# Kernel optimization log

Hardware: AMD Instinct MI355X
Metric: run time of the kernel (lower is better)

Reference implementation:

```python
import jax, jax.numpy as jnp
import numpy as np

D_MODEL = 1024
N_HEADS = 16
N_KV = 4
HEAD_DIM = D_MODEL // N_HEADS  # 64
EPS = 1e-5
THETA = 10000.0


def _rope_tables(S):
    half = HEAD_DIM // 2
    inv_freq = 1.0 / (THETA ** (jnp.arange(half, dtype=jnp.float32) / half))
    t = jnp.arange(S, dtype=jnp.float32)
    f = t[:, None] * inv_freq[None, :]  # [S, half]
    return jnp.cos(f), jnp.sin(f)


def _apply_rope(x, cos, sin):
    # x: [B, H, S, D]
    half = x.shape[-1] // 2
    x1, x2 = x[..., :half], x[..., half:]
    c = cos[None, None, :, :]
    s = sin[None, None, :, :]
    return jnp.concatenate([x1 * c - x2 * s, x1 * s + x2 * c], axis=-1)


def _rmsnorm(x, scale):
    rms = jnp.sqrt(jnp.mean(x * x, axis=-1, keepdims=True) + EPS)
    return x / rms * scale


def setup_inputs() -> dict:
    key = jax.random.key(0)
    ks = jax.random.split(key, 4)
    B, S = 2, 2048
    x = jax.random.normal(ks[0], (B, S, D_MODEL), dtype=jnp.float32)
    Wq = jax.random.normal(ks[1], (D_MODEL, D_MODEL), dtype=jnp.float32) * 0.02
    Wkv = jax.random.normal(ks[2], (D_MODEL, 2 * N_KV * HEAD_DIM), dtype=jnp.float32) * 0.02
    Wo = jax.random.normal(ks[3], (D_MODEL, D_MODEL), dtype=jnp.float32) * 0.02
    q_scale = jnp.ones((HEAD_DIM,), dtype=jnp.float32)
    k_scale = jnp.ones((HEAD_DIM,), dtype=jnp.float32)
    return {"x": x, "Wq": Wq, "Wkv": Wkv, "Wo": Wo,
            "q_scale": q_scale, "k_scale": k_scale}


def reference(x, Wq, Wkv, Wo, q_scale, k_scale):
    B, S, D = x.shape
    groups = N_HEADS // N_KV  # GQA group size

    # projections
    q = (x @ Wq).reshape(B, S, N_HEADS, HEAD_DIM).transpose(0, 2, 1, 3)  # [B,H,S,d]
    kv = x @ Wkv
    k, v = jnp.split(kv, 2, axis=-1)
    k = k.reshape(B, S, N_KV, HEAD_DIM).transpose(0, 2, 1, 3)  # [B,Hkv,S,d]
    v = v.reshape(B, S, N_KV, HEAD_DIM).transpose(0, 2, 1, 3)

    # per-head QK-RMSNorm (before RoPE, as in the torch module)
    q = _rmsnorm(q, q_scale)
    k = _rmsnorm(k, k_scale)

    # RoPE
    cos, sin = _rope_tables(S)
    q = _apply_rope(q, cos, sin)
    k = _apply_rope(k, cos, sin)

    # causal GQA attention (equivalent to SDPA with enable_gqa=True)
    qg = q.reshape(B, N_KV, groups, S, HEAD_DIM)
    scale = 1.0 / np.sqrt(HEAD_DIM).astype(np.float32)
    scores = jnp.einsum('bkgsd,bktd->bkgst', qg, k) * scale  # [B,Hkv,g,S,S]
    causal = jnp.tril(jnp.ones((S, S), dtype=bool))
    scores = jnp.where(causal[None, None, None], scores, -jnp.inf)
    attn = jax.nn.softmax(scores, axis=-1)
    out = jnp.einsum('bkgst,bktd->bkgsd', attn, v)
    out = out.reshape(B, N_HEADS, S, HEAD_DIM).transpose(0, 2, 1, 3).reshape(B, S, D)
    return out @ Wo
```

## Files before the change

kernel.cpp:

```cpp
#include <hip/hip_runtime.h>

#define S_LEN 2048
#define BATCH 2
#define DM    1024
#define NH    16
#define NKV   4
#define HD    64
#define MROWS (BATCH * S_LEN)
#define NQKV  1536

typedef __attribute__((ext_vector_type(8))) short bf16x8;
typedef __attribute__((ext_vector_type(4))) short s16x4;
typedef __attribute__((ext_vector_type(4))) float f32x4;
typedef __attribute__((ext_vector_type(4))) int i32x4;

__device__ __forceinline__ unsigned short f2bf(float f) {
  unsigned int u = __float_as_uint(f);
  u += 0x7FFF + ((u >> 16) & 1);
  return (unsigned short)(u >> 16);
}

__device__ __forceinline__ void gload_lds16(const unsigned short* g, unsigned short* l) {
  __builtin_amdgcn_global_load_lds((const __attribute__((address_space(1))) void*)g,
                                   (__attribute__((address_space(3))) void*)l, 16, 0, 0);
}
__device__ __forceinline__ void gload_lds4(const unsigned short* g, unsigned short* l) {
  __builtin_amdgcn_global_load_lds((const __attribute__((address_space(1))) void*)g,
                                   (__attribute__((address_space(3))) void*)l, 4, 0, 0);
}

__global__ __launch_bounds__(256) void prep_kernel(const float* __restrict__ x,
                                                   unsigned short* __restrict__ xb,
                                                   const float* __restrict__ Wq,
                                                   const float* __restrict__ Wkv,
                                                   const float* __restrict__ Wo,
                                                   unsigned short* __restrict__ wt1,
                                                   unsigned short* __restrict__ wot) {
  __shared__ float tile[64][65];
  int bid = blockIdx.x;
  int t = threadIdx.x;
  if (bid < 4096) {
    int i = (bid * 256 + t) * 4;
    float4 v = *reinterpret_cast<const float4*>(x + i);
    xb[i + 0] = f2bf(v.x);
    xb[i + 1] = f2bf(v.y);
    xb[i + 2] = f2bf(v.z);
    xb[i + 3] = f2bf(v.w);
    return;
  }
  bid -= 4096;
  const float* in;
  unsigned short* out;
  int C, bx, by;
  if (bid < 256) { in = Wq; out = wt1; C = 1024; bx = bid & 15; by = bid >> 4; }
  else if (bid < 384) { int k = bid - 256; in = Wkv; out = wt1 + 1024 * 1024; C = 512; bx = k & 7; by = k >> 3; }
  else { int k = bid - 384; in = Wo; out = wot; C = 1024; bx = k & 15; by = k >> 4; }
  const int R = 1024;
  int r0 = by * 64, c0 = bx * 64;
  int rl = t >> 2, cs = (t & 3) * 16;
#pragma unroll
  for (int k = 0; k < 4; ++k) {
    float4 v = *reinterpret_cast<const float4*>(in + (size_t)(r0 + rl) * C + c0 + cs + 4 * k);
    tile[rl][cs + 4 * k + 0] = v.x;
    tile[rl][cs + 4 * k + 1] = v.y;
    tile[rl][cs + 4 * k + 2] = v.z;
    tile[rl][cs + 4 * k + 3] = v.w;
  }
  __syncthreads();
  int cl = t >> 2, rs = (t & 3) * 16;
  bf16x8 v0, v1;
#pragma unroll
  for (int i = 0; i < 8; ++i) v0[i] = (short)f2bf(tile[rs + i][cl]);
#pragma unroll
  for (int i = 0; i < 8; ++i) v1[i] = (short)f2bf(tile[rs + 8 + i][cl]);
  unsigned short* dst = out + (size_t)(c0 + cl) * R + r0 + rs;
  *reinterpret_cast<bf16x8*>(dst) = v0;
  *reinterpret_cast<bf16x8*>(dst + 8) = v1;
}

__global__ __launch_bounds__(256) void gemm1_fused(const unsigned short* __restrict__ A,
                                                   const unsigned short* __restrict__ BT,
                                                   const float* __restrict__ q_scale,
                                                   const float* __restrict__ k_scale,
                                                   unsigned short* __restrict__ qb,
                                                   unsigned short* __restrict__ kbuf,
                                                   unsigned short* __restrict__ vt,
                                                   int K) {
  __shared__ __align__(16) unsigned short As[2][128 * 64];
  __shared__ __align__(16) unsigned short Bs[2][64 * 64];
  int bx = blockIdx.x;
  int row0 = blockIdx.y * 128, col0 = bx * 64;
  int t = threadIdx.x;
  int w = t >> 6, lane = t & 63, quad = lane >> 4, l16 = lane & 15;
  int srow = lane >> 3;
  int scol = (lane & 7) * 8;

  f32x4 acc[2][4];
#pragma unroll
  for (int i = 0; i < 2; ++i)
#pragma unroll
    for (int j = 0; j < 4; ++j) acc[i][j] = (f32x4){0.f, 0.f, 0.f, 0.f};

  auto stage = [&](int k0, int buf) {
#pragma unroll
    for (int j = 0; j < 4; ++j)
      gload_lds16(A + (size_t)(row0 + w * 32 + j * 8 + srow) * K + k0 + scol,
                  &As[buf][(w * 32 + j * 8) * 64]);
#pragma unroll
    for (int j = 0; j < 2; ++j)
      gload_lds16(BT + (size_t)(col0 + w * 16 + j * 8 + srow) * K + k0 + scol,
                  &Bs[buf][(w * 16 + j * 8) * 64]);
  };

  stage(0, 0);
  int cur = 0;
  for (int k0 = 0; k0 < K; k0 += 64) {
    __syncthreads();
    if (k0 + 64 < K) stage(k0 + 64, cur ^ 1);
#pragma unroll
    for (int ks = 0; ks < 2; ++ks) {
      bf16x8 af[2], bfr[4];
#pragma unroll
      for (int i = 0; i < 2; ++i)
        af[i] = *reinterpret_cast<const bf16x8*>(&As[cur][(w * 32 + i * 16 + l16) * 64 + ks * 32 + quad * 8]);
#pragma unroll
      for (int j = 0; j < 4; ++j)
        bfr[j] = *reinterpret_cast<const bf16x8*>(&Bs[cur][(j * 16 + l16) * 64 + ks * 32 + quad * 8]);
#pragma unroll
      for (int i = 0; i < 2; ++i)
#pragma unroll
        for (int j = 0; j < 4; ++j)
          acc[i][j] = __builtin_amdgcn_mfma_f32_16x16x32_bf16(af[i], bfr[j], acc[i][j], 0, 0, 0);
    }
    cur ^= 1;
  }

  if (bx < 20) {
    const float* scale = (bx < 16) ? q_scale : k_scale;
    float post = (bx < 16) ? 1.0f : 0.125f * 1.44269504088896f;
    float sc0 = scale[l16], sc1 = scale[16 + l16], sc2 = scale[32 + l16], sc3 = scale[48 + l16];
    float invf0 = exp2f((float)l16 * (-13.2877123795495f / 32.0f));
    float invf1 = exp2f((float)(l16 + 16) * (-13.2877123795495f / 32.0f));
#pragma unroll
    for (int i = 0; i < 2; ++i)
#pragma unroll
      for (int rg = 0; rg < 4; ++rg) {
        int row = row0 + w * 32 + i * 16 + quad * 4 + rg;
        int b = row >> 11, s = row & 2047;
        float v0 = acc[i][0][rg], v1 = acc[i][1][rg], v2 = acc[i][2][rg], v3 = acc[i][3][rg];
        float ss = v0 * v0 + v1 * v1 + v2 * v2 + v3 * v3;
        ss += __shfl_xor(ss, 1, 64);
        ss += __shfl_xor(ss, 2, 64);
        ss += __shfl_xor(ss, 4, 64);
        ss += __shfl_xor(ss, 8, 64);
        float inv_rms = 1.0f / sqrtf(ss * (1.0f / 64.0f) + 1e-5f);
        float n0 = v0 * inv_rms * sc0, n1 = v1 * inv_rms * sc1;
        float n2 = v2 * inv_rms * sc2, n3 = v3 * inv_rms * sc3;
        float f0 = (float)s * invf0, f1 = (float)s * invf1;
        float c0 = __cosf(f0), s0 = __sinf(f0), c1 = __cosf(f1), s1 = __sinf(f1);
        float o0 = (n0 * c0 - n2 * s0) * post;
        float o1 = (n1 * c1 - n3 * s1) * post;
        float o2 = (n0 * s0 + n2 * c0) * post;
        float o3 = (n1 * s1 + n3 * c1) * post;
        unsigned short* dst = (bx < 16)
            ? qb + ((size_t)(b * NH + bx) * S_LEN + s) * HD
            : kbuf + ((size_t)(b * NKV + (bx - 16)) * S_LEN + s) * HD;
        dst[l16] = f2bf(o0);
        dst[16 + l16] = f2bf(o1);
        dst[32 + l16] = f2bf(o2);
        dst[48 + l16] = f2bf(o3);
      }
  } else {
    int kvh = bx - 20;
    int b = row0 >> 11;
    unsigned short* vbase = vt + (size_t)(b * NKV + kvh) * HD * S_LEN;
#pragma unroll
    for (int i = 0; i < 2; ++i) {
      int s0 = (row0 & 2047) + w * 32 + i * 16 + quad * 4;
#pragma unroll
      for (int j = 0; j < 4; ++j) {
        int d = j * 16 + l16;
        s16x4 pv;
#pragma unroll
        for (int rg = 0; rg < 4; ++rg) pv[rg] = (short)f2bf(acc[i][j][rg]);
        *reinterpret_cast<s16x4*>(vbase + (size_t)d * S_LEN + s0) = pv;
      }
    }
  }
}

#define CH 136
#define TILE_SH (32 * CH)
__global__ __launch_bounds__(256, 4) void attn_kernel(const unsigned short* __restrict__ qb,
                                                      const unsigned short* __restrict__ kbuf,
                                                      const unsigned short* __restrict__ vt,
                                                      unsigned short* __restrict__ Opart,
                                                      float* __restrict__ lpart) {
  __shared__ __align__(16) unsigned short Ks[2][TILE_SH];
  __shared__ __align__(16) unsigned short Vs[2][TILE_SH];
  const size_t OZ = (size_t)BATCH * NH * S_LEN * HD;
  const size_t LZ = (size_t)BATCH * NH * S_LEN;
  int t32 = 63 - (int)(blockIdx.x >> 4);
  int sub = blockIdx.x & 15;
  int z = sub & 1;
  int bkv = sub >> 1;
  int b = bkv >> 2, kvh = bkv & 3;
  int w = threadIdx.x >> 6;
  int h = kvh * 4 + w;
  int lane = threadIdx.x & 63;
  int quad = lane >> 4, l16 = lane & 15;
  int qa = t32 * 32 + l16;
  const unsigned short* Q = qb + (size_t)(b * NH + h) * S_LEN * HD;
  const unsigned short* Kh = kbuf + (size_t)(b * NKV + kvh) * S_LEN * HD;
  const unsigned short* Vh = vt + (size_t)(b * NKV + kvh) * HD * S_LEN;

  bf16x8 bqa0 = *reinterpret_cast<const bf16x8*>(Q + (size_t)qa * HD + quad * 8);
  bf16x8 bqa1 = *reinterpret_cast<const bf16x8*>(Q + (size_t)qa * HD + 32 + quad * 8);
  bf16x8 bqb0 = *reinterpret_cast<const bf16x8*>(Q + (size_t)(qa + 16) * HD + quad * 8);
  bf16x8 bqb1 = *reinterpret_cast<const bf16x8*>(Q + (size_t)(qa + 16) * HD + 32 + quad * 8);

  bf16x8 ones;
#pragma unroll
  for (int i = 0; i < 8; ++i) ones[i] = (short)0x3F80;

  f32x4 ot[2][4];
#pragma unroll
  for (int gq = 0; gq < 2; ++gq)
#pragma unroll
    for (int i = 0; i < 4; ++i) ot[gq][i] = (f32x4){0.f, 0.f, 0.f, 0.f};
  f32x4 ol[2] = {(f32x4){0.f, 0.f, 0.f, 0.f}, (f32x4){0.f, 0.f, 0.f, 0.f}};

  int n = (t32 >> 1) + 1;

  auto stage = [&](int kbase, int dbuf) {
    const unsigned short* kg = Kh + (size_t)(kbase + w * 16) * HD + lane * 2;
    const unsigned short* vg = Vh + (size_t)(w * 16 + (lane >> 5)) * S_LEN + kbase + (lane & 31) * 2;
    unsigned short* kl = &Ks[dbuf][(w * 8) * CH];
    unsigned short* vl = &Vs[dbuf][(w * 8) * CH];
#pragma unroll
    for (int c = 0; c < 8; ++c) {
      gload_lds4(kg + (size_t)(2 * c) * HD, kl + c * CH);
      gload_lds4(vg + (size_t)(2 * c) * S_LEN, vl + c * CH);
    }
  };

  if (z < n) {
    stage(z << 6, 0);
    __syncthreads();

    for (int kb = z; kb < n; kb += 2) {
      int dbuf = (kb >> 1) & 1;
      bool diag = (kb == n - 1);
      if (kb + 2 < n) stage((kb + 2) << 6, dbuf ^ 1);
      int kbase = kb << 6;
      const unsigned short* Kd = Ks[dbuf];
      const unsigned short* Vd = Vs[dbuf];

      f32x4 sa[4], sb[4];
#pragma unroll
      for (int km = 0; km < 4; ++km) {
        int kk = 32 * (km >> 1) + 4 * (km & 1) + 8 * (l16 >> 2) + (l16 & 3);
        int base = (kk >> 1) * CH + (kk & 1) * 64;
        bf16x8 k0 = *reinterpret_cast<const bf16x8*>(&Kd[base + quad * 8]);
        bf16x8 k1 = *reinterpret_cast<const bf16x8*>(&Kd[base + 32 + quad * 8]);
        f32x4 s = {0.f, 0.f, 0.f, 0.f};
        s = __builtin_amdgcn_mfma_f32_16x16x32_bf16(k0, bqa0, s, 0, 0, 0);
        s = __builtin_amdgcn_mfma_f32_16x16x32_bf16(k1, bqa1, s, 0, 0, 0);
        sa[km] = s;
        f32x4 s2 = {0.f, 0.f, 0.f, 0.f};
        s2 = __builtin_amdgcn_mfma_f32_16x16x32_bf16(k0, bqb0, s2, 0, 0, 0);
        s2 = __builtin_amdgcn_mfma_f32_16x16x32_bf16(k1, bqb1, s2, 0, 0, 0);
        sb[km] = s2;
      }
      if (diag) {
#pragma unroll
        for (int km = 0; km < 4; ++km)
#pragma unroll
          for (int rg = 0; rg < 4; ++rg) {
            int key = kbase + 32 * (km >> 1) + 8 * quad + 4 * (km & 1) + rg;
            if (key > qa) sa[km][rg] = -1e30f;
            if (key > qa + 16) sb[km][rg] = -1e30f;
          }
      }
      unsigned int pk[4][2], qk[4][2];
#pragma unroll
      for (int km = 0; km < 4; ++km) {
        float a0 = exp2f(sa[km][0]), a1 = exp2f(sa[km][1]);
        float a2 = exp2f(sa[km][2]), a3 = exp2f(sa[km][3]);
        pk[km][0] = __builtin_amdgcn_perm(__float_as_uint(a1), __float_as_uint(a0), 0x07060302);
        pk[km][1] = __builtin_amdgcn_perm(__float_as_uint(a3), __float_as_uint(a2), 0x07060302);
        float b0 = exp2f(sb[km][0]), b1 = exp2f(sb[km][1]);
        float b2 = exp2f(sb[km][2]), b3 = exp2f(sb[km][3]);
        qk[km][0] = __builtin_amdgcn_perm(__float_as_uint(b1), __float_as_uint(b0), 0x07060302);
        qk[km][1] = __builtin_amdgcn_perm(__float_as_uint(b3), __float_as_uint(b2), 0x07060302);
      }
      i32x4 wa0 = {(int)pk[0][0], (int)pk[0][1], (int)pk[1][0], (int)pk[1][1]};
      i32x4 wa1 = {(int)pk[2][0], (int)pk[2][1], (int)pk[3][0], (int)pk[3][1]};
      i32x4 wb0 = {(int)qk[0][0], (int)qk[0][1], (int)qk[1][0], (int)qk[1][1]};
      i32x4 wb1 = {(int)qk[2][0], (int)qk[2][1], (int)qk[3][0], (int)qk[3][1]};
      bf16x8 pa0 = *reinterpret_cast<bf16x8*>(&wa0);
      bf16x8 pa1 = *reinterpret_cast<bf16x8*>(&wa1);
      bf16x8 pb0 = *reinterpret_cast<bf16x8*>(&wb0);
      bf16x8 pb1 = *reinterpret_cast<bf16x8*>(&wb1);
      ol[0] = __builtin_amdgcn_mfma_f32_16x16x32_bf16(ones, pa0, ol[0], 0, 0, 0);
      ol[0] = __builtin_amdgcn_mfma_f32_16x16x32_bf16(ones, pa1, ol[0], 0, 0, 0);
      ol[1] = __builtin_amdgcn_mfma_f32_16x16x32_bf16(ones, pb0, ol[1], 0, 0, 0);
      ol[1] = __builtin_amdgcn_mfma_f32_16x16x32_bf16(ones, pb1, ol[1], 0, 0, 0);
#pragma unroll
      for (int dm = 0; dm < 4; ++dm) {
        int ch = dm * 8 + (l16 >> 1);
        int base = ch * CH + (l16 & 1) * 64;
        bf16x8 v0 = *reinterpret_cast<const bf16x8*>(&Vd[base + quad * 8]);
        bf16x8 v1 = *reinterpret_cast<const bf16x8*>(&Vd[base + 32 + quad * 8]);
        ot[0][dm] = __builtin_amdgcn_mfma_f32_16x16x32_bf16(v0, pa0, ot[0][dm], 0, 0, 0);
        ot[0][dm] = __builtin_amdgcn_mfma_f32_16x16x32_bf16(v1, pa1, ot[0][dm], 0, 0, 0);
        ot[1][dm] = __builtin_amdgcn_mfma_f32_16x16x32_bf16(v0, pb0, ot[1][dm], 0, 0, 0);
        ot[1][dm] = __builtin_amdgcn_mfma_f32_16x16x32_bf16(v1, pb1, ot[1][dm], 0, 0, 0);
      }
      __syncthreads();
    }
  }

  unsigned short* Oz = Opart + (size_t)z * OZ;
  float* lz = lpart + (size_t)z * LZ;
#pragma unroll
  for (int gq = 0; gq < 2; ++gq) {
    size_t base = ((size_t)(b * NH + h) * S_LEN + qa + gq * 16) * HD;
#pragma unroll
    for (int dm = 0; dm < 4; ++dm) {
      s16x4 pv;
#pragma unroll
      for (int rg = 0; rg < 4; ++rg) pv[rg] = (short)f2bf(ot[gq][dm][rg]);
      *reinterpret_cast<s16x4*>(Oz + base + dm * 16 + quad * 4) = pv;
    }
  }
  if (quad == 0) {
    size_t lb = (size_t)(b * NH + h) * S_LEN + t32 * 32 + l16;
    lz[lb] = ol[0][0];
    lz[lb + 16] = ol[1][0];
  }
}

__global__ __launch_bounds__(256) void attn_combine_kernel(const unsigned short* __restrict__ Opart,
                                                           const float* __restrict__ lpart,
                                                           unsigned short* __restrict__ ctx) {
  const size_t OZ = (size_t)BATCH * NH * S_LEN * HD;
  const size_t LZ = (size_t)BATCH * NH * S_LEN;
  int i8 = blockIdx.x * 256 + threadIdx.x;
  size_t i = (size_t)i8 * 8;
  int row = i8 >> 3;
  bf16x8 a = *reinterpret_cast<const bf16x8*>(Opart + i);
  bf16x8 c = *reinterpret_cast<const bf16x8*>(Opart + OZ + i);
  float inv = 1.0f / (lpart[row] + lpart[LZ + row]);
  int q = row & 2047;
  int bh = row >> 11;
  int b = bh >> 4, h = bh & 15;
  int d0 = (i8 & 7) * 8;
  bf16x8 o;
#pragma unroll
  for (int k = 0; k < 8; ++k) {
    float fa = __uint_as_float(((unsigned int)(unsigned short)a[k]) << 16);
    float fc = __uint_as_float(((unsigned int)(unsigned short)c[k]) << 16);
    o[k] = (short)f2bf((fa + fc) * inv);
  }
  *reinterpret_cast<bf16x8*>(ctx + ((size_t)(b * S_LEN + q)) * DM + h * HD + d0) = o;
}

__global__ __launch_bounds__(256) void gemm_bt_n64(const unsigned short* __restrict__ A,
                                                   const unsigned short* __restrict__ BT,
                                                   float* __restrict__ C,
                                                   int M, int N, int K) {
  __shared__ __align__(16) unsigned short As[2][128 * 64];
  __shared__ __align__(16) unsigned short Bs[2][64 * 64];
  int row0 = blockIdx.y * 128, col0 = blockIdx.x * 64;
  int t = threadIdx.x;
  int w = t >> 6, lane = t & 63, quad = lane >> 4, l16 = lane & 15;
  int srow = lane >> 3;
  int scol = (lane & 7) * 8;

  f32x4 acc[2][4];
#pragma unroll
  for (int i = 0; i < 2; ++i)
#pragma unroll
    for (int j = 0; j < 4; ++j) acc[i][j] = (f32x4){0.f, 0.f, 0.f, 0.f};

  auto stage = [&](int k0, int buf) {
#pragma unroll
    for (int j = 0; j < 4; ++j)
      gload_lds16(A + (size_t)(row0 + w * 32 + j * 8 + srow) * K + k0 + scol,
                  &As[buf][(w * 32 + j * 8) * 64]);
#pragma unroll
    for (int j = 0; j < 2; ++j)
      gload_lds16(BT + (size_t)(col0 + w * 16 + j * 8 + srow) * K + k0 + scol,
                  &Bs[buf][(w * 16 + j * 8) * 64]);
  };

  stage(0, 0);
  int cur = 0;
  for (int k0 = 0; k0 < K; k0 += 64) {
    __syncthreads();
    if (k0 + 64 < K) stage(k0 + 64, cur ^ 1);
#pragma unroll
    for (int ks = 0; ks < 2; ++ks) {
      bf16x8 af[2], bfr[4];
#pragma unroll
      for (int i = 0; i < 2; ++i)
        af[i] = *reinterpret_cast<const bf16x8*>(&As[cur][(w * 32 + i * 16 + l16) * 64 + ks * 32 + quad * 8]);
#pragma unroll
      for (int j = 0; j < 4; ++j)
        bfr[j] = *reinterpret_cast<const bf16x8*>(&Bs[cur][(j * 16 + l16) * 64 + ks * 32 + quad * 8]);
#pragma unroll
      for (int i = 0; i < 2; ++i)
#pragma unroll
        for (int j = 0; j < 4; ++j)
          acc[i][j] = __builtin_amdgcn_mfma_f32_16x16x32_bf16(af[i], bfr[j], acc[i][j], 0, 0, 0);
    }
    cur ^= 1;
  }
#pragma unroll
  for (int i = 0; i < 2; ++i)
#pragma unroll
    for (int j = 0; j < 4; ++j) {
      int row = row0 + w * 32 + i * 16 + quad * 4;
      float* Cptr = C + (size_t)row * N + col0 + j * 16 + l16;
#pragma unroll
      for (int rg = 0; rg < 4; ++rg) Cptr[(size_t)rg * N] = acc[i][j][rg];
    }
}

extern "C" void kernel_launch(void* const* d_in, const int* in_sizes, int n_in,
                              void* d_out, int out_size, void* d_ws, size_t ws_size,
                              hipStream_t stream) {
  const float* x = (const float*)d_in[0];
  const float* Wq = (const float*)d_in[1];
  const float* Wkv = (const float*)d_in[2];
  const float* Wo = (const float*)d_in[3];
  const float* q_scale = (const float*)d_in[4];
  const float* k_scale = (const float*)d_in[5];
  float* out = (float*)d_out;

  char* ws = (char*)d_ws;
  size_t off = 0;
  auto alloc = [&](size_t bytes) {
    void* p = ws + off;
    off += (bytes + 255) & ~(size_t)255;
    return p;
  };
  unsigned short* xb = (unsigned short*)alloc((size_t)MROWS * DM * 2);
  unsigned short* wt1 = (unsigned short*)alloc((size_t)NQKV * DM * 2);
  unsigned short* wot = (unsigned short*)alloc((size_t)DM * DM * 2);
  unsigned short* qb = (unsigned short*)alloc((size_t)BATCH * NH * S_LEN * HD * 2);
  unsigned short* kbuf = (unsigned short*)alloc((size_t)BATCH * NKV * S_LEN * HD * 2);
  unsigned short* vt = (unsigned short*)alloc((size_t)BATCH * NKV * HD * S_LEN * 2);
  unsigned short* ctx = (unsigned short*)alloc((size_t)MROWS * DM * 2);
  unsigned short* Opart = (unsigned short*)alloc(2 * (size_t)BATCH * NH * S_LEN * HD * 2);
  float* lpart = (float*)alloc(2 * (size_t)BATCH * NH * S_LEN * 4);

  prep_kernel<<<4736, 256, 0, stream>>>(x, xb, Wq, Wkv, Wo, wt1, wot);

  gemm1_fused<<<dim3(NQKV / 64, MROWS / 128), 256, 0, stream>>>(xb, wt1, q_scale, k_scale,
                                                                qb, kbuf, vt, DM);

  attn_kernel<<<1024, 256, 0, stream>>>(qb, kbuf, vt, Opart, lpart);
  attn_combine_kernel<<<(BATCH * NH * S_LEN * HD / 8) / 256, 256, 0, stream>>>(Opart, lpart, ctx);

  gemm_bt_n64<<<dim3(DM / 64, MROWS / 128), 256, 0, stream>>>(ctx, wot, out, MROWS, DM, DM);
}
```

Measured before the change: 171.9 us.

## Drop split-K attention and fuse normalization into attention kernel epilogue

The attention kernel no longer splits each query tile's key range across two blocks. Each block now walks all key blocks with a single double-buffered pipeline and writes the normalized context directly, so the separate combine kernel and the partial O/l buffers go away. Blocks are ordered to pair heavy and light causal tiles (descending t32 for the first half, ascending for the second). The cost is half as many blocks (512) with longer serial loops per block, and launch bounds are relaxed to 2 blocks per SM, which could reduce parallelism on a large GPU.

Result: slower. 177.6 us (+3.3%).

```diff
diff --git a/kernel.cpp b/kernel.cpp
--- a/kernel.cpp
+++ b/kernel.cpp
@@ -191,19 +191,16 @@
 
 #define CH 136
 #define TILE_SH (32 * CH)
-__global__ __launch_bounds__(256, 4) void attn_kernel(const unsigned short* __restrict__ qb,
+__global__ __launch_bounds__(256, 2) void attn_kernel(const unsigned short* __restrict__ qb,
                                                       const unsigned short* __restrict__ kbuf,
                                                       const unsigned short* __restrict__ vt,
-                                                      unsigned short* __restrict__ Opart,
-                                                      float* __restrict__ lpart) {
+                                                      unsigned short* __restrict__ ctx) {
   __shared__ __align__(16) unsigned short Ks[2][TILE_SH];
   __shared__ __align__(16) unsigned short Vs[2][TILE_SH];
-  const size_t OZ = (size_t)BATCH * NH * S_LEN * HD;
-  const size_t LZ = (size_t)BATCH * NH * S_LEN;
-  int t32 = 63 - (int)(blockIdx.x >> 4);
-  int sub = blockIdx.x & 15;
-  int z = sub & 1;
-  int bkv = sub >> 1;
+  int bid = (int)blockIdx.x;
+  int u = bid >> 3;
+  int t32 = (bid < 256) ? (63 - 2 * u) : (2 * (u - 32));
+  int bkv = bid & 7;
   int b = bkv >> 2, kvh = bkv & 3;
   int w = threadIdx.x >> 6;
   int h = kvh * 4 + w;
@@ -244,126 +241,94 @@
     }
   };
 
-  if (z < n) {
-    stage(z << 6, 0);
+  stage(0, 0);
+  __syncthreads();
+
+  for (int kb = 0; kb < n; ++kb) {
+    int dbuf = kb & 1;
+    bool diag = (kb == n - 1);
+    if (kb + 1 < n) stage((kb + 1) << 6, dbuf ^ 1);
+    int kbase = kb << 6;
+    const unsigned short* Kd = Ks[dbuf];
+    const unsigned short* Vd = Vs[dbuf];
+
+    f32x4 sa[4], sb[4];
+#pragma unroll
+    for (int km = 0; km < 4; ++km) {
+      int kk = 32 * (km >> 1) + 4 * (km & 1) + 8 * (l16 >> 2) + (l16 & 3);
+      int base = (kk >> 1) * CH + (kk & 1) * 64;
+      bf16x8 k0 = *reinterpret_cast<const bf16x8*>(&Kd[base + quad * 8]);
+      bf16x8 k1 = *reinterpret_cast<const bf16x8*>(&Kd[base + 32 + quad * 8]);
+      f32x4 s = {0.f, 0.f, 0.f, 0.f};
+      s = __builtin_amdgcn_mfma_f32_16x16x32_bf16(k0, bqa0, s, 0, 0, 0);
+      s = __builtin_amdgcn_mfma_f32_16x16x32_bf16(k1, bqa1, s, 0, 0, 0);
+      sa[km] = s;
+      f32x4 s2 = {0.f, 0.f, 0.f, 0.f};
+      s2 = __builtin_amdgcn_mfma_f32_16x16x32_bf16(k0, bqb0, s2, 0, 0, 0);
+      s2 = __builtin_amdgcn_mfma_f32_16x16x32_bf16(k1, bqb1, s2, 0, 0, 0);
+      sb[km] = s2;
+    }
+    if (diag) {
+#pragma unroll
+      for (int km = 0; km < 4; ++km)
+#pragma unroll
+        for (int rg = 0; rg < 4; ++rg) {
+          int key = kbase + 32 * (km >> 1) + 8 * quad + 4 * (km & 1) + rg;
+          if (key > qa) sa[km][rg] = -1e30f;
+          if (key > qa + 16) sb[km][rg] = -1e30f;
+        }
+    }
+    unsigned int pk[4][2], qk[4][2];
+#pragma unroll
+    for (int km = 0; km < 4; ++km) {
+      float a0 = exp2f(sa[km][0]), a1 = exp2f(sa[km][1]);
+      float a2 = exp2f(sa[km][2]), a3 = exp2f(sa[km][3]);
+      pk[km][0] = __builtin_amdgcn_perm(__float_as_uint(a1), __float_as_uint(a0), 0x07060302);
+      pk[km][1] = __builtin_amdgcn_perm(__float_as_uint(a3), __float_as_uint(a2), 0x07060302);
+      float b0 = exp2f(sb[km][0]), b1 = exp2f(sb[km][1]);
+      float b2 = exp2f(sb[km][2]), b3 = exp2f(sb[km][3]);
+      qk[km][0] = __builtin_amdgcn_perm(__float_as_uint(b1), __float_as_uint(b0), 0x07060302);
+      qk[km][1] = __builtin_amdgcn_perm(__float_as_uint(b3), __float_as_uint(b2), 0x07060302);
+    }
+    i32x4 wa0 = {(int)pk[0][0], (int)pk[0][1], (int)pk[1][0], (int)pk[1][1]};
+    i32x4 wa1 = {(int)pk[2][0], (int)pk[2][1], (int)pk[3][0], (int)pk[3][1]};
+    i32x4 wb0 = {(int)qk[0][0], (int)qk[0][1], (int)qk[1][0], (int)qk[1][1]};
+    i32x4 wb1 = {(int)qk[2][0], (int)qk[2][1], (int)qk[3][0], (int)qk[3][1]};
+    bf16x8 pa0 = *reinterpret_cast<bf16x8*>(&wa0);
+    bf16x8 pa1 = *reinterpret_cast<bf16x8*>(&wa1);
+    bf16x8 pb0 = *reinterpret_cast<bf16x8*>(&wb0);
+    bf16x8 pb1 = *reinterpret_cast<bf16x8*>(&wb1);
+    ol[0] = __builtin_amdgcn_mfma_f32_16x16x32_bf16(ones, pa0, ol[0], 0, 0, 0);
+    ol[0] = __builtin_amdgcn_mfma_f32_16x16x32_bf16(ones, pa1, ol[0], 0, 0, 0);
+    ol[1] = __builtin_amdgcn_mfma_f32_16x16x32_bf16(ones, pb0, ol[1], 0, 0, 0);
+    ol[1] = __builtin_amdgcn_mfma_f32_16x16x32_bf16(ones, pb1, ol[1], 0, 0, 0);
+#pragma unroll
+    for (int dm = 0; dm < 4; ++dm) {
+      int ch = dm * 8 + (l16 >> 1);
+      int base = ch * CH + (l16 & 1) * 64;
+      bf16x8 v0 = *reinterpret_cast<const bf16x8*>(&Vd[base + quad * 8]);
+      bf16x8 v1 = *reinterpret_cast<const bf16x8*>(&Vd[base + 32 + quad * 8]);
+      ot[0][dm] = __builtin_amdgcn_mfma_f32_16x16x32_bf16(v0, pa0, ot[0][dm], 0, 0, 0);
+      ot[0][dm] = __builtin_amdgcn_mfma_f32_16x16x32_bf16(v1, pa1, ot[0][dm], 0, 0, 0);
+      ot[1][dm] = __builtin_amdgcn_mfma_f32_16x16x32_bf16(v0, pb0, ot[1][dm], 0, 0, 0);
+      ot[1][dm] = __builtin_amdgcn_mfma_f32_16x16x32_bf16(v1, pb1, ot[1][dm], 0, 0, 0);
+    }
     __syncthreads();
-
-    for (int kb = z; kb < n; kb += 2) {
-      int dbuf = (kb >> 1) & 1;
-      bool diag = (kb == n - 1);
-      if (kb + 2 < n) stage((kb + 2) << 6, dbuf ^ 1);
-      int kbase = kb << 6;
-      const unsigned short* Kd = Ks[dbuf];
-      const unsigned short* Vd = Vs[dbuf];
-
-      f32x4 sa[4], sb[4];
-#pragma unroll
-      for (int km = 0; km < 4; ++km) {
-        int kk = 32 * (km >> 1) + 4 * (km & 1) + 8 * (l16 >> 2) + (l16 & 3);
-        int base = (kk >> 1) * CH + (kk & 1) * 64;
-        bf16x8 k0 = *reinterpret_cast<const bf16x8*>(&Kd[base + quad * 8]);
-        bf16x8 k1 = *reinterpret_cast<const bf16x8*>(&Kd[base + 32 + quad * 8]);
-        f32x4 s = {0.f, 0.f, 0.f, 0.f};
-        s = __builtin_amdgcn_mfma_f32_16x16x32_bf16(k0, bqa0, s, 0, 0, 0);
-        s = __builtin_amdgcn_mfma_f32_16x16x32_bf16(k1, bqa1, s, 0, 0, 0);
-        sa[km] = s;
-        f32x4 s2 = {0.f, 0.f, 0.f, 0.f};
-        s2 = __builtin_amdgcn_mfma_f32_16x16x32_bf16(k0, bqb0, s2, 0, 0, 0);
-        s2 = __builtin_amdgcn_mfma_f32_16x16x32_bf16(k1, bqb1, s2, 0, 0, 0);
-        sb[km] = s2;
-      }
-      if (diag) {
-#pragma unroll
-        for (int km = 0; km < 4; ++km)
-#pragma unroll
-          for (int rg = 0; rg < 4; ++rg) {
-            int key = kbase + 32 * (km >> 1) + 8 * quad + 4 * (km & 1) + rg;
-            if (key > qa) sa[km][rg] = -1e30f;
-            if (key > qa + 16) sb[km][rg] = -1e30f;
-          }
-      }
-      unsigned int pk[4][2], qk[4][2];
-#pragma unroll
-      for (int km = 0; km < 4; ++km) {
-        float a0 = exp2f(sa[km][0]), a1 = exp2f(sa[km][1]);
-        float a2 = exp2f(sa[km][2]), a3 = exp2f(sa[km][3]);
-        pk[km][0] = __builtin_amdgcn_perm(__float_as_uint(a1), __float_as_uint(a0), 0x07060302);
-        pk[km][1] = __builtin_amdgcn_perm(__float_as_uint(a3), __float_as_uint(a2), 0x07060302);
-        float b0 = exp2f(sb[km][0]), b1 = exp2f(sb[km][1]);
-        float b2 = exp2f(sb[km][2]), b3 = exp2f(sb[km][3]);
-        qk[km][0] = __builtin_amdgcn_perm(__float_as_uint(b1), __float_as_uint(b0), 0x07060302);
-        qk[km][1] = __builtin_amdgcn_perm(__float_as_uint(b3), __float_as_uint(b2), 0x07060302);
-      }
-      i32x4 wa0 = {(int)pk[0][0], (int)pk[0][1], (int)pk[1][0], (int)pk[1][1]};
-      i32x4 wa1 = {(int)pk[2][0], (int)pk[2][1], (int)pk[3][0], (int)pk[3][1]};
-      i32x4 wb0 = {(int)qk[0][0], (int)qk[0][1], (int)qk[1][0], (int)qk[1][1]};
-      i32x4 wb1 = {(int)qk[2][0], (int)qk[2][1], (int)qk[3][0], (int)qk[3][1]};
-      bf16x8 pa0 = *reinterpret_cast<bf16x8*>(&wa0);
-      bf16x8 pa1 = *reinterpret_cast<bf16x8*>(&wa1);
-      bf16x8 pb0 = *reinterpret_cast<bf16x8*>(&wb0);
-      bf16x8 pb1 = *reinterpret_cast<bf16x8*>(&wb1);
-      ol[0] = __builtin_amdgcn_mfma_f32_16x16x32_bf16(ones, pa0, ol[0], 0, 0, 0);
-      ol[0] = __builtin_amdgcn_mfma_f32_16x16x32_bf16(ones, pa1, ol[0], 0, 0, 0);
-      ol[1] = __builtin_amdgcn_mfma_f32_16x16x32_bf16(ones, pb0, ol[1], 0, 0, 0);
-      ol[1] = __builtin_amdgcn_mfma_f32_16x16x32_bf16(ones, pb1, ol[1], 0, 0, 0);
-#pragma unroll
-      for (int dm = 0; dm < 4; ++dm) {
-        int ch = dm * 8 + (l16 >> 1);
-        int base = ch * CH + (l16 & 1) * 64;
-        bf16x8 v0 = *reinterpret_cast<const bf16x8*>(&Vd[base + quad * 8]);
-        bf16x8 v1 = *reinterpret_cast<const bf16x8*>(&Vd[base + 32 + quad * 8]);
-        ot[0][dm] = __builtin_amdgcn_mfma_f32_16x16x32_bf16(v0, pa0, ot[0][dm], 0, 0, 0);
-        ot[0][dm] = __builtin_amdgcn_mfma_f32_16x16x32_bf16(v1, pa1, ot[0][dm], 0, 0, 0);
-        ot[1][dm] = __builtin_amdgcn_mfma_f32_16x16x32_bf16(v0, pb0, ot[1][dm], 0, 0, 0);
-        ot[1][dm] = __builtin_amdgcn_mfma_f32_16x16x32_bf16(v1, pb1, ot[1][dm], 0, 0, 0);
-      }
-      __syncthreads();
-    }
-  }
-
-  unsigned short* Oz = Opart + (size_t)z * OZ;
-  float* lz = lpart + (size_t)z * LZ;
+  }
+
+  float inv[2] = {1.0f / ol[0][0], 1.0f / ol[1][0]};
 #pragma unroll
   for (int gq = 0; gq < 2; ++gq) {
-    size_t base = ((size_t)(b * NH + h) * S_LEN + qa + gq * 16) * HD;
+    int s = t32 * 32 + gq * 16 + l16;
+    unsigned short* dst = ctx + ((size_t)(b * S_LEN + s)) * DM + h * HD;
 #pragma unroll
     for (int dm = 0; dm < 4; ++dm) {
       s16x4 pv;
 #pragma unroll
-      for (int rg = 0; rg < 4; ++rg) pv[rg] = (short)f2bf(ot[gq][dm][rg]);
-      *reinterpret_cast<s16x4*>(Oz + base + dm * 16 + quad * 4) = pv;
-    }
-  }
-  if (quad == 0) {
-    size_t lb = (size_t)(b * NH + h) * S_LEN + t32 * 32 + l16;
-    lz[lb] = ol[0][0];
-    lz[lb + 16] = ol[1][0];
-  }
-}
-
-__global__ __launch_bounds__(256) void attn_combine_kernel(const unsigned short* __restrict__ Opart,
-                                                           const float* __restrict__ lpart,
-                                                           unsigned short* __restrict__ ctx) {
-  const size_t OZ = (size_t)BATCH * NH * S_LEN * HD;
-  const size_t LZ = (size_t)BATCH * NH * S_LEN;
-  int i8 = blockIdx.x * 256 + threadIdx.x;
-  size_t i = (size_t)i8 * 8;
-  int row = i8 >> 3;
-  bf16x8 a = *reinterpret_cast<const bf16x8*>(Opart + i);
-  bf16x8 c = *reinterpret_cast<const bf16x8*>(Opart + OZ + i);
-  float inv = 1.0f / (lpart[row] + lpart[LZ + row]);
-  int q = row & 2047;
-  int bh = row >> 11;
-  int b = bh >> 4, h = bh & 15;
-  int d0 = (i8 & 7) * 8;
-  bf16x8 o;
-#pragma unroll
-  for (int k = 0; k < 8; ++k) {
-    float fa = __uint_as_float(((unsigned int)(unsigned short)a[k]) << 16);
-    float fc = __uint_as_float(((unsigned int)(unsigned short)c[k]) << 16);
-    o[k] = (short)f2bf((fa + fc) * inv);
-  }
-  *reinterpret_cast<bf16x8*>(ctx + ((size_t)(b * S_LEN + q)) * DM + h * HD + d0) = o;
+      for (int rg = 0; rg < 4; ++rg) pv[rg] = (short)f2bf(ot[gq][dm][rg] * inv[gq]);
+      *reinterpret_cast<s16x4*>(dst + dm * 16 + quad * 4) = pv;
+    }
+  }
 }
 
 __global__ __launch_bounds__(256) void gemm_bt_n64(const unsigned short* __restrict__ A,
@@ -453,16 +418,13 @@
   unsigned short* kbuf = (unsigned short*)alloc((size_t)BATCH * NKV * S_LEN * HD * 2);
   unsigned short* vt = (unsigned short*)alloc((size_t)BATCH * NKV * HD * S_LEN * 2);
   unsigned short* ctx = (unsigned short*)alloc((size_t)MROWS * DM * 2);
-  unsigned short* Opart = (unsigned short*)alloc(2 * (size_t)BATCH * NH * S_LEN * HD * 2);
-  float* lpart = (float*)alloc(2 * (size_t)BATCH * NH * S_LEN * 4);
 
   prep_kernel<<<4736, 256, 0, stream>>>(x, xb, Wq, Wkv, Wo, wt1, wot);
 
   gemm1_fused<<<dim3(NQKV / 64, MROWS / 128), 256, 0, stream>>>(xb, wt1, q_scale, k_scale,
                                                                 qb, kbuf, vt, DM);
 
-  attn_kernel<<<1024, 256, 0, stream>>>(qb, kbuf, vt, Opart, lpart);
-  attn_combine_kernel<<<(BATCH * NH * S_LEN * HD / 8) / 256, 256, 0, stream>>>(Opart, lpart, ctx);
+  attn_kernel<<<512, 256, 0, stream>>>(qb, kbuf, vt, ctx);
 
   gemm_bt_n64<<<dim3(DM / 64, MROWS / 128), 256, 0, stream>>>(ctx, wot, out, MROWS, DM, DM);
 }
```
